# Optimization experiments

Hardware: AMD Instinct MI355X
Metric: run time of the kernel (lower is better)

The kernel has to match this reference:

```python
import jax, jax.numpy as jnp
import numpy as np

B, T, H, UNITS = 64, 512, 1024, 1024

def setup_inputs() -> dict:
    key = jax.random.key(0)
    ks = jax.random.split(key, 8)
    s = 0.02
    return {
        "dec_hidden": jax.random.normal(ks[0], (B, H), jnp.float32),
        "enc_output": jax.random.normal(ks[1], (B, T, H), jnp.float32),
        "Wh": jax.random.normal(ks[2], (H, UNITS), jnp.float32) * s,
        "bh": jnp.zeros((UNITS,), jnp.float32),
        "Ws": jax.random.normal(ks[3], (H, UNITS), jnp.float32) * s,
        "bs": jnp.zeros((UNITS,), jnp.float32),
        "Wv": jax.random.normal(ks[4], (UNITS, 1), jnp.float32) * s,
        "bv": jnp.zeros((1,), jnp.float32),
    }

def reference(dec_hidden, enc_output, Wh, bh, Ws, bs, Wv, bv):
    # Faithful to original: tanh applied only to W_h(enc_output) term.
    enc_proj = jnp.tanh(jnp.einsum('bth,hu->btu', enc_output, Wh) + bh)  # [B,T,U]
    dec_proj = (dec_hidden @ Ws + bs)[:, None, :]                        # [B,1,U]
    score = jnp.einsum('btu,uo->bto', enc_proj + dec_proj, Wv) + bv      # [B,T,1]
    attn_dist = jax.nn.softmax(score, axis=1)                            # [B,T,1]
    context_vector = jnp.sum(attn_dist * enc_output, axis=1)             # [B,H]
    return context_vector, jnp.squeeze(attn_dist, axis=-1)
```

## Files before the change

### kernel.cpp

```cpp
#include <hip/hip_runtime.h>
#include <hip/hip_bf16.h>

typedef unsigned short u16;
typedef __attribute__((ext_vector_type(8))) short short8;
typedef __attribute__((ext_vector_type(4))) float f32x4;

#define B_  64
#define T_  512
#define H_  1024
#define U_  1024
#define BT_ (B_*T_)

#define BM 128
#define BN 128
#define BK 32

#define GLL16(gp, lp) __builtin_amdgcn_global_load_lds( \
    (const __attribute__((address_space(1))) void*)(gp), \
    (__attribute__((address_space(3))) void*)(lp), 16, 0, 0)

__device__ __forceinline__ u16 f32_to_bf16(float f) {
  union { float f; unsigned u; } v; v.f = f;
  unsigned r = v.u + 0x7FFFu + ((v.u >> 16) & 1u);
  return (u16)(r >> 16);
}

__global__ __launch_bounds__(256) void ba_conv_enc(const float4* __restrict__ in,
                                                   ushort4* __restrict__ out) {
  int i = blockIdx.x * 256 + threadIdx.x;
  float4 v = in[i];
  ushort4 o;
  o.x = f32_to_bf16(v.x);
  o.y = f32_to_bf16(v.y);
  o.z = f32_to_bf16(v.z);
  o.w = f32_to_bf16(v.w);
  out[i] = o;
}

__global__ __launch_bounds__(256) void ba_conv_whT(const float* __restrict__ wh,
                                                   u16* __restrict__ whT) {
  __shared__ float tile[32][33];
  int tx = threadIdx.x, ty = threadIdx.y;
  int u0 = blockIdx.x * 32, h0 = blockIdx.y * 32;
  #pragma unroll
  for (int i = 0; i < 32; i += 8)
    tile[ty + i][tx] = wh[(long)(h0 + ty + i) * U_ + u0 + tx];
  __syncthreads();
  #pragma unroll
  for (int i = 0; i < 32; i += 8)
    whT[(long)(u0 + ty + i) * H_ + h0 + tx] = f32_to_bf16(tile[tx][ty + i]);
}

__global__ __launch_bounds__(256, 2) void ba_score(
    const u16* __restrict__ A, const u16* __restrict__ Bt,
    const float* __restrict__ bh, const float* __restrict__ wv,
    float* __restrict__ score) {
  __shared__ u16 lA[BM * BK];
  __shared__ u16 lB[BN * BK];

  const int tid  = threadIdx.x;
  const int wid  = tid >> 6;
  const int lane = tid & 63;
  const int wm = wid >> 1, wn = wid & 1;
  const long row0 = (long)blockIdx.x * BM;

  const int c0 = 2 * wid, c1 = 2 * wid + 1;
  const int lsub = lane >> 2;
  const int csub = (lane & 3) * 8;

  const int fr = lane & 15;
  const int ko = (lane >> 4) * 8;

  float sloc[4][4];
  #pragma unroll
  for (int i = 0; i < 4; ++i)
    #pragma unroll
    for (int r = 0; r < 4; ++r) sloc[i][r] = 0.f;

  const int ntBase = blockIdx.y * 4;
  for (int nt = ntBase; nt < ntBase + 4; ++nt) {
    const int ncol0 = nt * BN;
    f32x4 acc[4][4];
    #pragma unroll
    for (int i = 0; i < 4; ++i)
      #pragma unroll
      for (int j = 0; j < 4; ++j) acc[i][j] = (f32x4){0.f, 0.f, 0.f, 0.f};

    for (int kt = 0; kt < H_; kt += BK) {
      GLL16(A + (row0 + 16 * c0 + lsub) * H_ + kt + csub, (char*)lA + c0 * 1024);
      GLL16(A + (row0 + 16 * c1 + lsub) * H_ + kt + csub, (char*)lA + c1 * 1024);
      GLL16(Bt + (long)(ncol0 + 16 * c0 + lsub) * H_ + kt + csub, (char*)lB + c0 * 1024);
      GLL16(Bt + (long)(ncol0 + 16 * c1 + lsub) * H_ + kt + csub, (char*)lB + c1 * 1024);
      __syncthreads();

      short8 av[4], bv[4];
      #pragma unroll
      for (int i = 0; i < 4; ++i) {
        av[i] = *(const short8*)&lA[(wm * 64 + i * 16 + fr) * BK + ko];
        bv[i] = *(const short8*)&lB[(wn * 64 + i * 16 + fr) * BK + ko];
      }
      #pragma unroll
      for (int i = 0; i < 4; ++i)
        #pragma unroll
        for (int j = 0; j < 4; ++j)
          acc[i][j] = __builtin_amdgcn_mfma_f32_16x16x32_bf16(av[i], bv[j], acc[i][j], 0, 0, 0);
      __syncthreads();
    }

    #pragma unroll
    for (int j = 0; j < 4; ++j) {
      const int n = ncol0 + wn * 64 + j * 16 + fr;
      const float bhn = bh[n];
      const float wvn = wv[n];
      #pragma unroll
      for (int i = 0; i < 4; ++i) {
        #pragma unroll
        for (int r = 0; r < 4; ++r) {
          float x = acc[i][j][r] + bhn;
          float e = __expf(2.f * x);
          float t = 1.f - 2.f / (e + 1.f);
          sloc[i][r] += t * wvn;
        }
      }
    }
  }

  #pragma unroll
  for (int i = 0; i < 4; ++i) {
    #pragma unroll
    for (int r = 0; r < 4; ++r) {
      float v = sloc[i][r];
      v += __shfl_xor(v, 1);
      v += __shfl_xor(v, 2);
      v += __shfl_xor(v, 4);
      v += __shfl_xor(v, 8);
      if ((lane & 15) == 0) {
        int m = wm * 64 + i * 16 + (lane >> 4) * 4 + r;
        atomicAdd(&score[row0 + m], v);
      }
    }
  }
}

__global__ __launch_bounds__(256) void ba_softmax(const float* __restrict__ score,
                                                  float* __restrict__ attn) {
  int b = blockIdx.x, tid = threadIdx.x;
  int lane = tid & 63, wid = tid >> 6;
  const float* s = score + b * T_;
  float v0 = s[tid], v1 = s[tid + 256];
  float m = fmaxf(v0, v1);
  #pragma unroll
  for (int o = 1; o < 64; o <<= 1) m = fmaxf(m, __shfl_xor(m, o));
  __shared__ float redm[4];
  __shared__ float reds[4];
  if (lane == 0) redm[wid] = m;
  __syncthreads();
  m = fmaxf(fmaxf(redm[0], redm[1]), fmaxf(redm[2], redm[3]));
  float e0 = __expf(v0 - m), e1 = __expf(v1 - m);
  float sum = e0 + e1;
  #pragma unroll
  for (int o = 1; o < 64; o <<= 1) sum += __shfl_xor(sum, o);
  if (lane == 0) reds[wid] = sum;
  __syncthreads();
  float tot = reds[0] + reds[1] + reds[2] + reds[3];
  float inv = 1.f / tot;
  attn[b * T_ + tid] = e0 * inv;
  attn[b * T_ + tid + 256] = e1 * inv;
}

__global__ __launch_bounds__(256) void ba_context(const float* __restrict__ enc,
                                                  const float* __restrict__ attn,
                                                  float* __restrict__ ctx) {
  int b = blockIdx.y;
  int h = blockIdx.x * 256 + threadIdx.x;
  const float* e = enc + (long)b * T_ * H_ + h;
  const float* a = attn + b * T_;
  float acc = 0.f;
  #pragma unroll 8
  for (int t = 0; t < T_; ++t) acc = fmaf(a[t], e[(long)t * H_], acc);
  ctx[(long)b * H_ + h] = acc;
}

extern "C" void kernel_launch(void* const* d_in, const int* in_sizes, int n_in,
                              void* d_out, int out_size, void* d_ws, size_t ws_size,
                              hipStream_t stream) {
  const float* enc = (const float*)d_in[1];
  const float* Wh  = (const float*)d_in[2];
  const float* bh  = (const float*)d_in[3];
  const float* Wv  = (const float*)d_in[6];

  float* out      = (float*)d_out;
  float* ctx_out  = out;
  float* attn_out = out + B_ * H_;

  char* ws = (char*)d_ws;
  u16*  encb  = (u16*)ws;
  u16*  whT   = (u16*)(ws + (size_t)67108864);
  float* score = (float*)(ws + (size_t)67108864 + 2097152);

  ba_conv_enc<<<BT_ * H_ / 4 / 256, 256, 0, stream>>>((const float4*)enc, (ushort4*)encb);
  ba_conv_whT<<<dim3(U_ / 32, H_ / 32), dim3(32, 8), 0, stream>>>(Wh, whT);
  hipMemsetAsync(score, 0, BT_ * sizeof(float), stream);
  ba_score<<<dim3(BT_ / BM, 2), 256, 0, stream>>>(encb, whT, bh, Wv, score);
  ba_softmax<<<B_, 256, 0, stream>>>(score, attn_out);
  ba_context<<<dim3(H_ / 256, B_), 256, 0, stream>>>(enc, attn_out, ctx_out);
}
```

Baseline: 345.5 us.

## Swizzle LDS tiles, one N-tile per score block, split-T context with atomics

The score GEMM now gives each block a single 128-column N tile, which raises the grid to 2048 blocks, and it raises the occupancy hint to 4 blocks per CU. An XOR-style swizzle on the LDS column offset is meant to remove bank conflicts on the fragment reads. The context kernel is split over T chunks with float4 loads and atomicAdd into a zeroed output, and the enc conversion now writes 16-byte stores. The cost is more atomics and more tail work per block, plus nondeterministic summation order in the context output.

```diff
diff --git a/kernel.cpp b/kernel.cpp
--- a/kernel.cpp
+++ b/kernel.cpp
@@ -24,16 +24,19 @@
   unsigned r = v.u + 0x7FFFu + ((v.u >> 16) & 1u);
   return (u16)(r >> 16);
 }
+__device__ __forceinline__ unsigned pack_bf16x2(float lo, float hi) {
+  return (unsigned)f32_to_bf16(lo) | ((unsigned)f32_to_bf16(hi) << 16);
+}
 
 __global__ __launch_bounds__(256) void ba_conv_enc(const float4* __restrict__ in,
-                                                   ushort4* __restrict__ out) {
+                                                   uint4* __restrict__ out) {
   int i = blockIdx.x * 256 + threadIdx.x;
-  float4 v = in[i];
-  ushort4 o;
-  o.x = f32_to_bf16(v.x);
-  o.y = f32_to_bf16(v.y);
-  o.z = f32_to_bf16(v.z);
-  o.w = f32_to_bf16(v.w);
+  float4 v0 = in[2 * i], v1 = in[2 * i + 1];
+  uint4 o;
+  o.x = pack_bf16x2(v0.x, v0.y);
+  o.y = pack_bf16x2(v0.z, v0.w);
+  o.z = pack_bf16x2(v1.x, v1.y);
+  o.w = pack_bf16x2(v1.z, v1.w);
   out[i] = o;
 }
 
@@ -51,7 +54,7 @@
     whT[(long)(u0 + ty + i) * H_ + h0 + tx] = f32_to_bf16(tile[tx][ty + i]);
 }
 
-__global__ __launch_bounds__(256, 2) void ba_score(
+__global__ __launch_bounds__(256, 4) void ba_score(
     const u16* __restrict__ A, const u16* __restrict__ Bt,
     const float* __restrict__ bh, const float* __restrict__ wv,
     float* __restrict__ score) {
@@ -62,65 +65,62 @@
   const int wid  = tid >> 6;
   const int lane = tid & 63;
   const int wm = wid >> 1, wn = wid & 1;
-  const long row0 = (long)blockIdx.x * BM;
+  const long row0  = (long)blockIdx.x * BM;
+  const int  ncol0 = blockIdx.y * BN;
 
   const int c0 = 2 * wid, c1 = 2 * wid + 1;
   const int lsub = lane >> 2;
-  const int csub = (lane & 3) * 8;
+  const int csw = (((lane & 3) - ((lane >> 3) & 3)) & 3) * 8;
 
   const int fr = lane & 15;
-  const int ko = (lane >> 4) * 8;
-
-  float sloc[4][4];
+  const int pofs = ((((lane >> 4) + ((lane >> 1) & 3)) & 3)) * 8;
+
+  f32x4 acc[4][4];
   #pragma unroll
   for (int i = 0; i < 4; ++i)
     #pragma unroll
-    for (int r = 0; r < 4; ++r) sloc[i][r] = 0.f;
-
-  const int ntBase = blockIdx.y * 4;
-  for (int nt = ntBase; nt < ntBase + 4; ++nt) {
-    const int ncol0 = nt * BN;
-    f32x4 acc[4][4];
+    for (int j = 0; j < 4; ++j) acc[i][j] = (f32x4){0.f, 0.f, 0.f, 0.f};
+
+  for (int kt = 0; kt < H_; kt += BK) {
+    GLL16(A + (row0 + 16 * c0 + lsub) * H_ + kt + csw, (char*)lA + c0 * 1024);
+    GLL16(A + (row0 + 16 * c1 + lsub) * H_ + kt + csw, (char*)lA + c1 * 1024);
+    GLL16(Bt + (long)(ncol0 + 16 * c0 + lsub) * H_ + kt + csw, (char*)lB + c0 * 1024);
+    GLL16(Bt + (long)(ncol0 + 16 * c1 + lsub) * H_ + kt + csw, (char*)lB + c1 * 1024);
+    __syncthreads();
+
+    short8 av[4], bvv[4];
+    #pragma unroll
+    for (int i = 0; i < 4; ++i) {
+      av[i]  = *(const short8*)&lA[(wm * 64 + i * 16 + fr) * BK + pofs];
+      bvv[i] = *(const short8*)&lB[(wn * 64 + i * 16 + fr) * BK + pofs];
+    }
     #pragma unroll
     for (int i = 0; i < 4; ++i)
       #pragma unroll
-      for (int j = 0; j < 4; ++j) acc[i][j] = (f32x4){0.f, 0.f, 0.f, 0.f};
-
-    for (int kt = 0; kt < H_; kt += BK) {
-      GLL16(A + (row0 + 16 * c0 + lsub) * H_ + kt + csub, (char*)lA + c0 * 1024);
-      GLL16(A + (row0 + 16 * c1 + lsub) * H_ + kt + csub, (char*)lA + c1 * 1024);
-      GLL16(Bt + (long)(ncol0 + 16 * c0 + lsub) * H_ + kt + csub, (char*)lB + c0 * 1024);
-      GLL16(Bt + (long)(ncol0 + 16 * c1 + lsub) * H_ + kt + csub, (char*)lB + c1 * 1024);
-      __syncthreads();
-
-      short8 av[4], bv[4];
+      for (int j = 0; j < 4; ++j)
+        acc[i][j] = __builtin_amdgcn_mfma_f32_16x16x32_bf16(av[i], bvv[j], acc[i][j], 0, 0, 0);
+    __syncthreads();
+  }
+
+  float sloc[4][4];
+  #pragma unroll
+  for (int i = 0; i < 4; ++i)
+    #pragma unroll
+    for (int r = 0; r < 4; ++r) sloc[i][r] = 0.f;
+
+  #pragma unroll
+  for (int j = 0; j < 4; ++j) {
+    const int n = ncol0 + wn * 64 + j * 16 + fr;
+    const float bhn = bh[n];
+    const float wvn = wv[n];
+    #pragma unroll
+    for (int i = 0; i < 4; ++i) {
       #pragma unroll
-      for (int i = 0; i < 4; ++i) {
-        av[i] = *(const short8*)&lA[(wm * 64 + i * 16 + fr) * BK + ko];
-        bv[i] = *(const short8*)&lB[(wn * 64 + i * 16 + fr) * BK + ko];
-      }
-      #pragma unroll
-      for (int i = 0; i < 4; ++i)
-        #pragma unroll
-        for (int j = 0; j < 4; ++j)
-          acc[i][j] = __builtin_amdgcn_mfma_f32_16x16x32_bf16(av[i], bv[j], acc[i][j], 0, 0, 0);
-      __syncthreads();
-    }
-
-    #pragma unroll
-    for (int j = 0; j < 4; ++j) {
-      const int n = ncol0 + wn * 64 + j * 16 + fr;
-      const float bhn = bh[n];
-      const float wvn = wv[n];
-      #pragma unroll
-      for (int i = 0; i < 4; ++i) {
-        #pragma unroll
-        for (int r = 0; r < 4; ++r) {
-          float x = acc[i][j][r] + bhn;
-          float e = __expf(2.f * x);
-          float t = 1.f - 2.f / (e + 1.f);
-          sloc[i][r] += t * wvn;
-        }
+      for (int r = 0; r < 4; ++r) {
+        float x = acc[i][j][r] + bhn;
+        float e = __expf(2.f * x);
+        float t = 1.f - 2.f / (e + 1.f);
+        sloc[i][r] += t * wvn;
       }
     }
   }
@@ -168,17 +168,29 @@
   attn[b * T_ + tid + 256] = e1 * inv;
 }
 
-__global__ __launch_bounds__(256) void ba_context(const float* __restrict__ enc,
+__global__ __launch_bounds__(256) void ba_context(const float4* __restrict__ enc4,
                                                   const float* __restrict__ attn,
                                                   float* __restrict__ ctx) {
-  int b = blockIdx.y;
-  int h = blockIdx.x * 256 + threadIdx.x;
-  const float* e = enc + (long)b * T_ * H_ + h;
-  const float* a = attn + b * T_;
-  float acc = 0.f;
-  #pragma unroll 8
-  for (int t = 0; t < T_; ++t) acc = fmaf(a[t], e[(long)t * H_], acc);
-  ctx[(long)b * H_ + h] = acc;
+  int b = blockIdx.x;
+  int t0 = blockIdx.y * 32;
+  int tid = threadIdx.x;
+  const float4* e = enc4 + ((long)b * T_ + t0) * (H_ / 4) + tid;
+  const float* a = attn + b * T_ + t0;
+  float4 acc = {0.f, 0.f, 0.f, 0.f};
+  #pragma unroll 4
+  for (int t = 0; t < 32; ++t) {
+    float4 v = e[(long)t * (H_ / 4)];
+    float at = a[t];
+    acc.x = fmaf(at, v.x, acc.x);
+    acc.y = fmaf(at, v.y, acc.y);
+    acc.z = fmaf(at, v.z, acc.z);
+    acc.w = fmaf(at, v.w, acc.w);
+  }
+  float* c = ctx + b * H_ + tid * 4;
+  atomicAdd(c + 0, acc.x);
+  atomicAdd(c + 1, acc.y);
+  atomicAdd(c + 2, acc.z);
+  atomicAdd(c + 3, acc.w);
 }
 
 extern "C" void kernel_launch(void* const* d_in, const int* in_sizes, int n_in,
@@ -194,14 +206,15 @@
   float* attn_out = out + B_ * H_;
 
   char* ws = (char*)d_ws;
-  u16*  encb  = (u16*)ws;
-  u16*  whT   = (u16*)(ws + (size_t)67108864);
+  u16*  encb   = (u16*)ws;
+  u16*  whT    = (u16*)(ws + (size_t)67108864);
   float* score = (float*)(ws + (size_t)67108864 + 2097152);
 
-  ba_conv_enc<<<BT_ * H_ / 4 / 256, 256, 0, stream>>>((const float4*)enc, (ushort4*)encb);
+  ba_conv_enc<<<BT_ * H_ / 8 / 256, 256, 0, stream>>>((const float4*)enc, (uint4*)encb);
   ba_conv_whT<<<dim3(U_ / 32, H_ / 32), dim3(32, 8), 0, stream>>>(Wh, whT);
   hipMemsetAsync(score, 0, BT_ * sizeof(float), stream);
-  ba_score<<<dim3(BT_ / BM, 2), 256, 0, stream>>>(encb, whT, bh, Wv, score);
+  hipMemsetAsync(ctx_out, 0, B_ * H_ * sizeof(float), stream);
+  ba_score<<<dim3(BT_ / BM, U_ / BN), 256, 0, stream>>>(encb, whT, bh, Wv, score);
   ba_softmax<<<B_, 256, 0, stream>>>(score, attn_out);
-  ba_context<<<dim3(H_ / 256, B_), 256, 0, stream>>>(enc, attn_out, ctx_out);
-}
+  ba_context<<<dim3(B_, 16), 256, 0, stream>>>((const float4*)enc, attn_out, ctx_out);
+}
```

Result: no change. 344.5 us (-0.3%).
